# Performance work log

Hardware: AMD Instinct MI355X
Metric: run time of the kernel (lower is better)

Reference implementation:

```python
import jax, jax.numpy as jnp
import numpy as np

IN_CH = 256
BOT = IN_CH // 2  # bottleneck channels
B, W, H = 4, 64, 64


def setup_inputs() -> dict:
    key = jax.random.key(0)
    ks = jax.random.split(key, 10)
    s_in = 1.0 / np.sqrt(IN_CH)   # torch Conv2d default init scale (kaiming-ish bound)
    s_bt = 1.0 / np.sqrt(BOT)
    return {
        "X": jax.random.normal(ks[0], (B, IN_CH, W, H), dtype=jnp.float32),
        "Wq": jax.random.uniform(ks[1], (BOT, IN_CH), jnp.float32, -s_in, s_in),
        "bq": jax.random.uniform(ks[2], (BOT,), jnp.float32, -s_in, s_in),
        "Wk": jax.random.uniform(ks[3], (BOT, IN_CH), jnp.float32, -s_in, s_in),
        "bk": jax.random.uniform(ks[4], (BOT,), jnp.float32, -s_in, s_in),
        "Wv": jax.random.uniform(ks[5], (BOT, IN_CH), jnp.float32, -s_in, s_in),
        "bv": jax.random.uniform(ks[6], (BOT,), jnp.float32, -s_in, s_in),
        "Wo": jax.random.uniform(ks[7], (IN_CH, BOT), jnp.float32, -s_bt, s_bt),
        "bo": jax.random.uniform(ks[8], (IN_CH,), jnp.float32, -s_bt, s_bt),
        "gamma": 0.1 * jax.random.normal(ks[9], (1,), dtype=jnp.float32),
    }


def reference(X, Wq, bq, Wk, bk, Wv, bv, Wo, bo, gamma):
    b, c, w, h = X.shape
    n = w * h
    Xf = X.reshape(b, c, n)  # [b, c, n] — 1x1 conv == per-pixel linear
    q = jnp.einsum('oc,bcn->bon', Wq, Xf) + bq[None, :, None]  # [b, c/2, n]
    k = jnp.einsum('oc,bcn->bon', Wk, Xf) + bk[None, :, None]
    v = jnp.einsum('oc,bcn->bon', Wv, Xf) + bv[None, :, None]
    # score[b,i,j] = sum_c q[b,c,i] * k[b,c,j]; softmax over dim=1 (query index i)
    score = jnp.einsum('bci,bcj->bij', q, k)          # [b, n, n]
    attn = jax.nn.softmax(score, axis=1)
    out = jnp.einsum('bci,bij->bcj', v, attn)         # [b, c/2, n]
    out = jnp.einsum('oc,bcn->bon', Wo, out) + bo[None, :, None]  # [b, c, n]
    out = out.reshape(b, c, w, h)
    return gamma[0] * out + X
```

## Files before the change

### kernel.cpp

```cpp
#include <hip/hip_runtime.h>
#include <math.h>

#define NBATCH 4
#define CIN    256
#define CBOT   128
#define NPIX   4096
#define NPART  4
#define LOG2E  1.44269504f

typedef __attribute__((ext_vector_type(4))) float f32x4;
typedef __attribute__((ext_vector_type(8))) short bf16x8;

__device__ __forceinline__ unsigned short f2bf(float f) {
    union { float f; unsigned u; } v; v.f = f;
    unsigned r = (v.u + 0x7FFFu + ((v.u >> 16) & 1u)) >> 16;
    return (unsigned short)r;
}
__device__ __forceinline__ float bf2f(unsigned short h) {
    union { unsigned u; float f; } v; v.u = ((unsigned)h) << 16; return v.f;
}
__device__ __forceinline__ bf16x8 pack8(const float* s) {
    bf16x8 r;
#pragma unroll
    for (int t = 0; t < 8; ++t) r[t] = (short)f2bf(s[t]);
    return r;
}

__global__ __launch_bounds__(256) void k_xt(
    const float* __restrict__ X, unsigned short* __restrict__ Xt)
{
    __shared__ float T[64][65];
    const int tid = threadIdx.x;
    const int pbase = blockIdx.x * 64;
    const int c0    = blockIdx.y * 64;
    const int b     = blockIdx.z;
#pragma unroll
    for (int k = 0; k < 4; ++k) {
        int f = tid + 256 * k;
        int cl = f >> 4, p4 = (f & 15) << 2;
        float4 v = *(const float4*)(X + (size_t)b * CIN * NPIX + (size_t)(c0 + cl) * NPIX + pbase + p4);
        T[cl][p4 + 0] = v.x; T[cl][p4 + 1] = v.y;
        T[cl][p4 + 2] = v.z; T[cl][p4 + 3] = v.w;
    }
    __syncthreads();
#pragma unroll
    for (int k = 0; k < 4; ++k) {
        int f = tid + 256 * k;
        int p = f >> 4, c4 = (f & 15) << 2;
        ushort4 u;
        u.x = f2bf(T[c4 + 0][p]); u.y = f2bf(T[c4 + 1][p]);
        u.z = f2bf(T[c4 + 2][p]); u.w = f2bf(T[c4 + 3][p]);
        *(ushort4*)&Xt[((size_t)b * NPIX + pbase + p) * CIN + c0 + c4] = u;
    }
}

__global__ __launch_bounds__(256) void k_qkv(
    const unsigned short* __restrict__ Xt,
    const float* __restrict__ Wq, const float* __restrict__ bq,
    const float* __restrict__ Wk, const float* __restrict__ bk,
    const float* __restrict__ Wv, const float* __restrict__ bv,
    unsigned short* __restrict__ Qt, unsigned short* __restrict__ Kt,
    unsigned short* __restrict__ Vt)
{
    const int tid = threadIdx.x;
    const int wv = tid >> 6, lane = tid & 63;
    const int grp = lane & 15, quad = lane >> 4;
    const int pbase = blockIdx.x * 64;
    const int b     = blockIdx.y;
    const unsigned short* __restrict__ Xb = Xt + (size_t)b * NPIX * CIN;
    const int obase = 32 * wv;

    f32x4 aQ[2][4], aK[2][4], aV[4][2];
#pragma unroll
    for (int mt = 0; mt < 2; ++mt)
#pragma unroll
        for (int nt = 0; nt < 4; ++nt) { aQ[mt][nt] = (f32x4)0.f; aK[mt][nt] = (f32x4)0.f; }
#pragma unroll
    for (int mt = 0; mt < 4; ++mt)
#pragma unroll
        for (int nt = 0; nt < 2; ++nt) aV[mt][nt] = (f32x4)0.f;

    for (int ks = 0; ks < 8; ++ks) {
        bf16x8 bx[4];
#pragma unroll
        for (int nt = 0; nt < 4; ++nt)
            bx[nt] = *(const bf16x8*)&Xb[(size_t)(pbase + nt * 16 + grp) * CIN + ks * 32 + quad * 8];
        bf16x8 wq_[2], wk_[2], wv_[2];
#pragma unroll
        for (int mt = 0; mt < 2; ++mt) {
            const size_t roff = (size_t)(obase + mt * 16 + grp) * CIN + ks * 32 + quad * 8;
            float w8[8];
            *(float4*)&w8[0] = *(const float4*)(Wq + roff);
            *(float4*)&w8[4] = *(const float4*)(Wq + roff + 4);
            wq_[mt] = pack8(w8);
            *(float4*)&w8[0] = *(const float4*)(Wk + roff);
            *(float4*)&w8[4] = *(const float4*)(Wk + roff + 4);
            wk_[mt] = pack8(w8);
            *(float4*)&w8[0] = *(const float4*)(Wv + roff);
            *(float4*)&w8[4] = *(const float4*)(Wv + roff + 4);
            wv_[mt] = pack8(w8);
        }
#pragma unroll
        for (int mt = 0; mt < 2; ++mt)
#pragma unroll
            for (int nt = 0; nt < 4; ++nt) {
                aQ[mt][nt] = __builtin_amdgcn_mfma_f32_16x16x32_bf16(wq_[mt], bx[nt], aQ[mt][nt], 0, 0, 0);
                aK[mt][nt] = __builtin_amdgcn_mfma_f32_16x16x32_bf16(wk_[mt], bx[nt], aK[mt][nt], 0, 0, 0);
            }
#pragma unroll
        for (int mt = 0; mt < 4; ++mt)
#pragma unroll
            for (int nt = 0; nt < 2; ++nt)
                aV[mt][nt] = __builtin_amdgcn_mfma_f32_16x16x32_bf16(bx[mt], wv_[nt], aV[mt][nt], 0, 0, 0);
    }

    unsigned short* Qb_ = Qt + (size_t)b * NPIX * CBOT;
    unsigned short* Kb_ = Kt + (size_t)b * NPIX * CBOT;
#pragma unroll
    for (int mt = 0; mt < 2; ++mt) {
        int o0 = obase + mt * 16 + quad * 4;
        float b4q[4], b4k[4];
#pragma unroll
        for (int r = 0; r < 4; ++r) { b4q[r] = bq[o0 + r]; b4k[r] = bk[o0 + r]; }
#pragma unroll
        for (int nt = 0; nt < 4; ++nt) {
            int p = pbase + nt * 16 + grp;
            ushort4 uq, uk;
            uq.x = f2bf(aQ[mt][nt][0] + b4q[0]); uq.y = f2bf(aQ[mt][nt][1] + b4q[1]);
            uq.z = f2bf(aQ[mt][nt][2] + b4q[2]); uq.w = f2bf(aQ[mt][nt][3] + b4q[3]);
            uk.x = f2bf((aK[mt][nt][0] + b4k[0]) * LOG2E);
            uk.y = f2bf((aK[mt][nt][1] + b4k[1]) * LOG2E);
            uk.z = f2bf((aK[mt][nt][2] + b4k[2]) * LOG2E);
            uk.w = f2bf((aK[mt][nt][3] + b4k[3]) * LOG2E);
            *(ushort4*)&Qb_[(size_t)p * CBOT + o0] = uq;
            *(ushort4*)&Kb_[(size_t)p * CBOT + o0] = uk;
        }
    }
    unsigned short* Vb_ = Vt + (size_t)b * CBOT * NPIX;
#pragma unroll
    for (int nt = 0; nt < 2; ++nt) {
        int o = obase + nt * 16 + grp;
        float bb = bv[o];
#pragma unroll
        for (int mt = 0; mt < 4; ++mt) {
            int p0 = pbase + mt * 16 + quad * 4;
            ushort4 u;
            u.x = f2bf(aV[mt][nt][0] + bb); u.y = f2bf(aV[mt][nt][1] + bb);
            u.z = f2bf(aV[mt][nt][2] + bb); u.w = f2bf(aV[mt][nt][3] + bb);
            *(ushort4*)&Vb_[(size_t)o * NPIX + p0] = u;
        }
    }
}

__global__ __launch_bounds__(256, 2) void k_flash(
    const unsigned short* __restrict__ Qt,
    const unsigned short* __restrict__ Kt,
    const unsigned short* __restrict__ Vt,
    unsigned short* __restrict__ Opart,
    float* __restrict__ Lpart)
{
    __shared__ __align__(16) unsigned short Qs[64][136];
    __shared__ __align__(16) unsigned short Vs[128][72];
    __shared__ __align__(16) unsigned short Ps[128][72];
    const int tid  = threadIdx.x;
    const int wv   = tid >> 6, lane = tid & 63;
    const int grp  = lane & 15, quad = lane >> 4;
    const int jblk = blockIdx.x * 128;
    const int part = blockIdx.y;
    const int b    = blockIdx.z;
    const int tbeg = part * (64 / NPART);
    const int tend = tbeg + (64 / NPART);
    const unsigned short* __restrict__ Qb = Qt + (size_t)b * NPIX * CBOT;
    const unsigned short* __restrict__ Kb = Kt + (size_t)b * NPIX * CBOT;
    const unsigned short* __restrict__ Vb = Vt + (size_t)b * CBOT * NPIX;

    bf16x8 aq[2][4];
#pragma unroll
    for (int set = 0; set < 2; ++set)
#pragma unroll
        for (int ks = 0; ks < 4; ++ks)
            aq[set][ks] = *(const bf16x8*)&Kb[
                (size_t)(jblk + wv * 32 + set * 16 + grp) * CBOT + ks * 32 + quad * 8];

    bf16x8 bones;
#pragma unroll
    for (int t = 0; t < 8; ++t) bones[t] = (short)0x3F80;

    f32x4 o[2][8];
#pragma unroll
    for (int set = 0; set < 2; ++set)
#pragma unroll
        for (int ct = 0; ct < 8; ++ct) o[set][ct] = (f32x4)0.f;
    f32x4 lacc[2] = {(f32x4)0.f, (f32x4)0.f};

    const int qrow = tid >> 4,          qch = tid & 15;
    const int vrow = tid >> 3,          vch = tid & 7;
    bf16x8 qreg[4], vreg[4];
#pragma unroll
    for (int k = 0; k < 4; ++k) {
        qreg[k] = *(const bf16x8*)&Qb[(size_t)(tbeg * 64 + qrow + 16 * k) * CBOT + qch * 8];
        vreg[k] = *(const bf16x8*)&Vb[(size_t)(vrow + 32 * k) * NPIX + tbeg * 64 + vch * 8];
    }

    for (int it = tbeg; it < tend; ++it) {
        __syncthreads();
#pragma unroll
        for (int k = 0; k < 4; ++k) {
            *(bf16x8*)&Qs[qrow + 16 * k][qch * 8] = qreg[k];
            *(bf16x8*)&Vs[vrow + 32 * k][vch * 8] = vreg[k];
        }
        __syncthreads();
        if (it + 1 < tend) {
            const int i1 = (it + 1) * 64;
#pragma unroll
            for (int k = 0; k < 4; ++k) {
                qreg[k] = *(const bf16x8*)&Qb[(size_t)(i1 + qrow + 16 * k) * CBOT + qch * 8];
                vreg[k] = *(const bf16x8*)&Vb[(size_t)(vrow + 32 * k) * NPIX + i1 + vch * 8];
            }
        }

        f32x4 sf[2][4];
#pragma unroll
        for (int set = 0; set < 2; ++set)
#pragma unroll
            for (int nt = 0; nt < 4; ++nt) sf[set][nt] = (f32x4)0.f;
#pragma unroll
        for (int nt = 0; nt < 4; ++nt)
#pragma unroll
            for (int ks = 0; ks < 4; ++ks) {
                bf16x8 bq_ = *(const bf16x8*)&Qs[nt * 16 + grp][ks * 32 + quad * 8];
                sf[0][nt] = __builtin_amdgcn_mfma_f32_16x16x32_bf16(aq[0][ks], bq_, sf[0][nt], 0, 0, 0);
                sf[1][nt] = __builtin_amdgcn_mfma_f32_16x16x32_bf16(aq[1][ks], bq_, sf[1][nt], 0, 0, 0);
            }

#pragma unroll
        for (int set = 0; set < 2; ++set)
#pragma unroll
            for (int nt = 0; nt < 4; ++nt)
#pragma unroll
                for (int r = 0; r < 4; ++r)
                    Ps[wv * 32 + set * 16 + quad * 4 + r][nt * 16 + grp] =
                        f2bf(exp2f(sf[set][nt][r]));

        bf16x8 af[2][2];
#pragma unroll
        for (int set = 0; set < 2; ++set)
#pragma unroll
            for (int ks2 = 0; ks2 < 2; ++ks2)
                af[set][ks2] = *(const bf16x8*)&Ps[wv * 32 + set * 16 + grp][ks2 * 32 + quad * 8];

#pragma unroll
        for (int ct = 0; ct < 8; ++ct)
#pragma unroll
            for (int ks2 = 0; ks2 < 2; ++ks2) {
                bf16x8 bv_ = *(const bf16x8*)&Vs[ct * 16 + grp][ks2 * 32 + quad * 8];
                o[0][ct] = __builtin_amdgcn_mfma_f32_16x16x32_bf16(af[0][ks2], bv_, o[0][ct], 0, 0, 0);
                o[1][ct] = __builtin_amdgcn_mfma_f32_16x16x32_bf16(af[1][ks2], bv_, o[1][ct], 0, 0, 0);
            }
#pragma unroll
        for (int set = 0; set < 2; ++set) {
            lacc[set] = __builtin_amdgcn_mfma_f32_16x16x32_bf16(af[set][0], bones, lacc[set], 0, 0, 0);
            lacc[set] = __builtin_amdgcn_mfma_f32_16x16x32_bf16(af[set][1], bones, lacc[set], 0, 0, 0);
        }
    }

    unsigned short* Ob = Opart + ((size_t)(part * NBATCH + b) * NPIX + jblk) * CBOT;
#pragma unroll
    for (int set = 0; set < 2; ++set)
#pragma unroll
        for (int ct = 0; ct < 8; ++ct)
#pragma unroll
            for (int r = 0; r < 4; ++r)
                Ob[(size_t)(wv * 32 + set * 16 + quad * 4 + r) * CBOT + ct * 16 + grp] =
                    f2bf(o[set][ct][r]);
    if (grp == 0) {
#pragma unroll
        for (int set = 0; set < 2; ++set)
#pragma unroll
            for (int r = 0; r < 4; ++r)
                Lpart[(size_t)(part * NBATCH + b) * NPIX + jblk + wv * 32 + set * 16 + quad * 4 + r] =
                    lacc[set][r];
    }
}

__global__ __launch_bounds__(256) void k_oproj(
    const unsigned short* __restrict__ Opart, const float* __restrict__ Lpart,
    const float* __restrict__ Wo, const float* __restrict__ bo,
    const float* __restrict__ gamma, const float* __restrict__ X,
    float* __restrict__ Out)
{
    const int tid = threadIdx.x;
    const int wv = tid >> 6, lane = tid & 63;
    const int grp = lane & 15, quad = lane >> 4;
    const int pbase = blockIdx.x * 32;
    const int b     = blockIdx.y;
    const int obase = 64 * wv;

    f32x4 acc[2][4];
#pragma unroll
    for (int mt = 0; mt < 2; ++mt)
#pragma unroll
        for (int nt = 0; nt < 4; ++nt) acc[mt][nt] = (f32x4)0.f;

    for (int ks = 0; ks < 4; ++ks) {
        bf16x8 ao[2];
#pragma unroll
        for (int mt = 0; mt < 2; ++mt) {
            int p = pbase + mt * 16 + grp;
            float s[8] = {0.f, 0.f, 0.f, 0.f, 0.f, 0.f, 0.f, 0.f};
#pragma unroll
            for (int part = 0; part < NPART; ++part) {
                bf16x8 u = *(const bf16x8*)&Opart[
                    ((size_t)(part * NBATCH + b) * NPIX + p) * CBOT + ks * 32 + quad * 8];
#pragma unroll
                for (int t = 0; t < 8; ++t) s[t] += bf2f((unsigned short)u[t]);
            }
            ao[mt] = pack8(s);
        }
        bf16x8 bw[4];
#pragma unroll
        for (int nt = 0; nt < 4; ++nt) {
            const float* wp = Wo + (size_t)(obase + nt * 16 + grp) * CBOT + ks * 32 + quad * 8;
            float w8[8];
            *(float4*)&w8[0] = *(const float4*)wp;
            *(float4*)&w8[4] = *(const float4*)(wp + 4);
            bw[nt] = pack8(w8);
        }
#pragma unroll
        for (int mt = 0; mt < 2; ++mt)
#pragma unroll
            for (int nt = 0; nt < 4; ++nt)
                acc[mt][nt] = __builtin_amdgcn_mfma_f32_16x16x32_bf16(ao[mt], bw[nt], acc[mt][nt], 0, 0, 0);
    }

    float linv[2][4];
#pragma unroll
    for (int mt = 0; mt < 2; ++mt)
#pragma unroll
        for (int r = 0; r < 4; ++r) {
            int p = pbase + mt * 16 + quad * 4 + r;
            float ls = 0.f;
#pragma unroll
            for (int part = 0; part < NPART; ++part)
                ls += Lpart[(size_t)(part * NBATCH + b) * NPIX + p];
            linv[mt][r] = 1.f / ls;
        }
    float g = gamma[0];
#pragma unroll
    for (int nt = 0; nt < 4; ++nt) {
        int o = obase + nt * 16 + grp;
        float bb = bo[o];
#pragma unroll
        for (int mt = 0; mt < 2; ++mt) {
            int p0 = pbase + mt * 16 + quad * 4;
            size_t base = (size_t)b * CIN * NPIX + (size_t)o * NPIX + p0;
            float4 x4 = *(const float4*)(X + base);
            float4 r4;
            r4.x = g * (acc[mt][nt][0] * linv[mt][0] + bb) + x4.x;
            r4.y = g * (acc[mt][nt][1] * linv[mt][1] + bb) + x4.y;
            r4.z = g * (acc[mt][nt][2] * linv[mt][2] + bb) + x4.z;
            r4.w = g * (acc[mt][nt][3] * linv[mt][3] + bb) + x4.w;
            *(float4*)(Out + base) = r4;
        }
    }
}

extern "C" void kernel_launch(void* const* d_in, const int* in_sizes, int n_in,
                              void* d_out, int out_size, void* d_ws, size_t ws_size,
                              hipStream_t stream)
{
    (void)in_sizes; (void)n_in; (void)out_size; (void)ws_size;
    const float* X     = (const float*)d_in[0];
    const float* Wq    = (const float*)d_in[1];
    const float* bq    = (const float*)d_in[2];
    const float* Wk    = (const float*)d_in[3];
    const float* bk    = (const float*)d_in[4];
    const float* Wv    = (const float*)d_in[5];
    const float* bv    = (const float*)d_in[6];
    const float* Wo    = (const float*)d_in[7];
    const float* bo    = (const float*)d_in[8];
    const float* gamma = (const float*)d_in[9];
    float* out = (float*)d_out;

    const size_t BNC = (size_t)NBATCH * NPIX * CBOT;
    unsigned short* Qt    = (unsigned short*)d_ws;
    unsigned short* Kt    = Qt + BNC;
    unsigned short* Vt    = Kt + BNC;
    unsigned short* Opart = Vt + BNC;
    unsigned short* Xt    = Opart;
    float*          Lpart = (float*)(Opart + (size_t)NPART * BNC);

    k_xt   <<<dim3(64, 4, NBATCH),     256, 0, stream>>>(X, Xt);
    k_qkv  <<<dim3(64, NBATCH),        256, 0, stream>>>(Xt, Wq, bq, Wk, bk, Wv, bv, Qt, Kt, Vt);
    k_flash<<<dim3(32, NPART, NBATCH), 256, 0, stream>>>(Qt, Kt, Vt, Opart, Lpart);
    k_oproj<<<dim3(128, NBATCH),       256, 0, stream>>>(Opart, Lpart, Wo, bo, gamma, X, out);
}
```

Before: 177.1 us.

## Pre-convert weights to bf16 once, halve qkv pixel tile, skip partial summation

```diff
diff --git a/kernel.cpp b/kernel.cpp
--- a/kernel.cpp
+++ b/kernel.cpp
@@ -16,14 +16,21 @@
     unsigned r = (v.u + 0x7FFFu + ((v.u >> 16) & 1u)) >> 16;
     return (unsigned short)r;
 }
-__device__ __forceinline__ float bf2f(unsigned short h) {
-    union { unsigned u; float f; } v; v.u = ((unsigned)h) << 16; return v.f;
-}
-__device__ __forceinline__ bf16x8 pack8(const float* s) {
-    bf16x8 r;
-#pragma unroll
-    for (int t = 0; t < 8; ++t) r[t] = (short)f2bf(s[t]);
-    return r;
+
+__global__ __launch_bounds__(256) void k_wcvt(
+    const float* __restrict__ Wq, const float* __restrict__ Wk,
+    const float* __restrict__ Wv, const float* __restrict__ Wo,
+    unsigned short* __restrict__ Wb)
+{
+    const int f4 = (blockIdx.x * 256 + threadIdx.x) * 4;
+    const int reg = f4 >> 15, loc = f4 & 32767;
+    const float* __restrict__ W = (reg == 0) ? Wq : (reg == 1) ? Wk : (reg == 2) ? Wv : Wo;
+    const float sc = (reg == 1) ? LOG2E : 1.f;
+    float4 v = *(const float4*)(W + loc);
+    ushort4 u;
+    u.x = f2bf(v.x * sc); u.y = f2bf(v.y * sc);
+    u.z = f2bf(v.z * sc); u.w = f2bf(v.w * sc);
+    *(ushort4*)&Wb[f4] = u;
 }
 
 __global__ __launch_bounds__(256) void k_xt(
@@ -56,62 +63,52 @@
 
 __global__ __launch_bounds__(256) void k_qkv(
     const unsigned short* __restrict__ Xt,
-    const float* __restrict__ Wq, const float* __restrict__ bq,
-    const float* __restrict__ Wk, const float* __restrict__ bk,
-    const float* __restrict__ Wv, const float* __restrict__ bv,
+    const unsigned short* __restrict__ Wb,
+    const float* __restrict__ bq, const float* __restrict__ bk,
+    const float* __restrict__ bv,
     unsigned short* __restrict__ Qt, unsigned short* __restrict__ Kt,
     unsigned short* __restrict__ Vt)
 {
     const int tid = threadIdx.x;
     const int wv = tid >> 6, lane = tid & 63;
     const int grp = lane & 15, quad = lane >> 4;
-    const int pbase = blockIdx.x * 64;
+    const int pbase = blockIdx.x * 32;
     const int b     = blockIdx.y;
-    const unsigned short* __restrict__ Xb = Xt + (size_t)b * NPIX * CIN;
+    const unsigned short* __restrict__ Xb  = Xt + (size_t)b * NPIX * CIN;
+    const unsigned short* __restrict__ Wqb = Wb;
+    const unsigned short* __restrict__ Wkb = Wb + 32768;
+    const unsigned short* __restrict__ Wvb = Wb + 65536;
     const int obase = 32 * wv;
 
-    f32x4 aQ[2][4], aK[2][4], aV[4][2];
+    f32x4 aQ[2][2], aK[2][2], aV[2][2];
 #pragma unroll
     for (int mt = 0; mt < 2; ++mt)
 #pragma unroll
-        for (int nt = 0; nt < 4; ++nt) { aQ[mt][nt] = (f32x4)0.f; aK[mt][nt] = (f32x4)0.f; }
-#pragma unroll
-    for (int mt = 0; mt < 4; ++mt)
-#pragma unroll
-        for (int nt = 0; nt < 2; ++nt) aV[mt][nt] = (f32x4)0.f;
+        for (int nt = 0; nt < 2; ++nt) {
+            aQ[mt][nt] = (f32x4)0.f; aK[mt][nt] = (f32x4)0.f; aV[mt][nt] = (f32x4)0.f;
+        }
 
     for (int ks = 0; ks < 8; ++ks) {
-        bf16x8 bx[4];
-#pragma unroll
-        for (int nt = 0; nt < 4; ++nt)
+        bf16x8 bx[2];
+#pragma unroll
+        for (int nt = 0; nt < 2; ++nt)
             bx[nt] = *(const bf16x8*)&Xb[(size_t)(pbase + nt * 16 + grp) * CIN + ks * 32 + quad * 8];
         bf16x8 wq_[2], wk_[2], wv_[2];
 #pragma unroll
         for (int mt = 0; mt < 2; ++mt) {
             const size_t roff = (size_t)(obase + mt * 16 + grp) * CIN + ks * 32 + quad * 8;
-            float w8[8];
-            *(float4*)&w8[0] = *(const float4*)(Wq + roff);
-            *(float4*)&w8[4] = *(const float4*)(Wq + roff + 4);
-            wq_[mt] = pack8(w8);
-            *(float4*)&w8[0] = *(const float4*)(Wk + roff);
-            *(float4*)&w8[4] = *(const float4*)(Wk + roff + 4);
-            wk_[mt] = pack8(w8);
-            *(float4*)&w8[0] = *(const float4*)(Wv + roff);
-            *(float4*)&w8[4] = *(const float4*)(Wv + roff + 4);
-            wv_[mt] = pack8(w8);
+            wq_[mt] = *(const bf16x8*)&Wqb[roff];
+            wk_[mt] = *(const bf16x8*)&Wkb[roff];
+            wv_[mt] = *(const bf16x8*)&Wvb[roff];
         }
 #pragma unroll
         for (int mt = 0; mt < 2; ++mt)
 #pragma unroll
-            for (int nt = 0; nt < 4; ++nt) {
+            for (int nt = 0; nt < 2; ++nt) {
                 aQ[mt][nt] = __builtin_amdgcn_mfma_f32_16x16x32_bf16(wq_[mt], bx[nt], aQ[mt][nt], 0, 0, 0);
                 aK[mt][nt] = __builtin_amdgcn_mfma_f32_16x16x32_bf16(wk_[mt], bx[nt], aK[mt][nt], 0, 0, 0);
-            }
-#pragma unroll
-        for (int mt = 0; mt < 4; ++mt)
-#pragma unroll
-            for (int nt = 0; nt < 2; ++nt)
                 aV[mt][nt] = __builtin_amdgcn_mfma_f32_16x16x32_bf16(bx[mt], wv_[nt], aV[mt][nt], 0, 0, 0);
+            }
     }
 
     unsigned short* Qb_ = Qt + (size_t)b * NPIX * CBOT;
@@ -121,17 +118,15 @@
         int o0 = obase + mt * 16 + quad * 4;
         float b4q[4], b4k[4];
 #pragma unroll
-        for (int r = 0; r < 4; ++r) { b4q[r] = bq[o0 + r]; b4k[r] = bk[o0 + r]; }
-#pragma unroll
-        for (int nt = 0; nt < 4; ++nt) {
+        for (int r = 0; r < 4; ++r) { b4q[r] = bq[o0 + r]; b4k[r] = bk[o0 + r] * LOG2E; }
+#pragma unroll
+        for (int nt = 0; nt < 2; ++nt) {
             int p = pbase + nt * 16 + grp;
             ushort4 uq, uk;
             uq.x = f2bf(aQ[mt][nt][0] + b4q[0]); uq.y = f2bf(aQ[mt][nt][1] + b4q[1]);
             uq.z = f2bf(aQ[mt][nt][2] + b4q[2]); uq.w = f2bf(aQ[mt][nt][3] + b4q[3]);
-            uk.x = f2bf((aK[mt][nt][0] + b4k[0]) * LOG2E);
-            uk.y = f2bf((aK[mt][nt][1] + b4k[1]) * LOG2E);
-            uk.z = f2bf((aK[mt][nt][2] + b4k[2]) * LOG2E);
-            uk.w = f2bf((aK[mt][nt][3] + b4k[3]) * LOG2E);
+            uk.x = f2bf(aK[mt][nt][0] + b4k[0]); uk.y = f2bf(aK[mt][nt][1] + b4k[1]);
+            uk.z = f2bf(aK[mt][nt][2] + b4k[2]); uk.w = f2bf(aK[mt][nt][3] + b4k[3]);
             *(ushort4*)&Qb_[(size_t)p * CBOT + o0] = uq;
             *(ushort4*)&Kb_[(size_t)p * CBOT + o0] = uk;
         }
@@ -142,7 +137,7 @@
         int o = obase + nt * 16 + grp;
         float bb = bv[o];
 #pragma unroll
-        for (int mt = 0; mt < 4; ++mt) {
+        for (int mt = 0; mt < 2; ++mt) {
             int p0 = pbase + mt * 16 + quad * 4;
             ushort4 u;
             u.x = f2bf(aV[mt][nt][0] + bb); u.y = f2bf(aV[mt][nt][1] + bb);
@@ -193,8 +188,8 @@
         for (int ct = 0; ct < 8; ++ct) o[set][ct] = (f32x4)0.f;
     f32x4 lacc[2] = {(f32x4)0.f, (f32x4)0.f};
 
-    const int qrow = tid >> 4,          qch = tid & 15;
-    const int vrow = tid >> 3,          vch = tid & 7;
+    const int qrow = tid >> 4, qch = tid & 15;
+    const int vrow = tid >> 3, vch = tid & 7;
     bf16x8 qreg[4], vreg[4];
 #pragma unroll
     for (int k = 0; k < 4; ++k) {
@@ -285,7 +280,7 @@
 
 __global__ __launch_bounds__(256) void k_oproj(
     const unsigned short* __restrict__ Opart, const float* __restrict__ Lpart,
-    const float* __restrict__ Wo, const float* __restrict__ bo,
+    const unsigned short* __restrict__ Wob, const float* __restrict__ bo,
     const float* __restrict__ gamma, const float* __restrict__ X,
     float* __restrict__ Out)
 {
@@ -303,34 +298,22 @@
         for (int nt = 0; nt < 4; ++nt) acc[mt][nt] = (f32x4)0.f;
 
     for (int ks = 0; ks < 4; ++ks) {
-        bf16x8 ao[2];
+        bf16x8 bw[4];
+#pragma unroll
+        for (int nt = 0; nt < 4; ++nt)
+            bw[nt] = *(const bf16x8*)&Wob[(size_t)(obase + nt * 16 + grp) * CBOT + ks * 32 + quad * 8];
 #pragma unroll
         for (int mt = 0; mt < 2; ++mt) {
             int p = pbase + mt * 16 + grp;
-            float s[8] = {0.f, 0.f, 0.f, 0.f, 0.f, 0.f, 0.f, 0.f};
 #pragma unroll
             for (int part = 0; part < NPART; ++part) {
-                bf16x8 u = *(const bf16x8*)&Opart[
+                bf16x8 ao = *(const bf16x8*)&Opart[
                     ((size_t)(part * NBATCH + b) * NPIX + p) * CBOT + ks * 32 + quad * 8];
 #pragma unroll
-                for (int t = 0; t < 8; ++t) s[t] += bf2f((unsigned short)u[t]);
-            }
-            ao[mt] = pack8(s);
-        }
-        bf16x8 bw[4];
-#pragma unroll
-        for (int nt = 0; nt < 4; ++nt) {
-            const float* wp = Wo + (size_t)(obase + nt * 16 + grp) * CBOT + ks * 32 + quad * 8;
-            float w8[8];
-            *(float4*)&w8[0] = *(const float4*)wp;
-            *(float4*)&w8[4] = *(const float4*)(wp + 4);
-            bw[nt] = pack8(w8);
-        }
-#pragma unroll
-        for (int mt = 0; mt < 2; ++mt)
-#pragma unroll
-            for (int nt = 0; nt < 4; ++nt)
-                acc[mt][nt] = __builtin_amdgcn_mfma_f32_16x16x32_bf16(ao[mt], bw[nt], acc[mt][nt], 0, 0, 0);
+                for (int nt = 0; nt < 4; ++nt)
+                    acc[mt][nt] = __builtin_amdgcn_mfma_f32_16x16x32_bf16(ao, bw[nt], acc[mt][nt], 0, 0, 0);
+            }
+        }
     }
 
     float linv[2][4];
@@ -389,9 +372,11 @@
     unsigned short* Opart = Vt + BNC;
     unsigned short* Xt    = Opart;
     float*          Lpart = (float*)(Opart + (size_t)NPART * BNC);
-
+    unsigned short* Wb    = (unsigned short*)(Lpart + (size_t)NPART * NBATCH * NPIX);
+
+    k_wcvt <<<dim3(128),               256, 0, stream>>>(Wq, Wk, Wv, Wo, Wb);
     k_xt   <<<dim3(64, 4, NBATCH),     256, 0, stream>>>(X, Xt);
-    k_qkv  <<<dim3(64, NBATCH),        256, 0, stream>>>(Xt, Wq, bq, Wk, bk, Wv, bv, Qt, Kt, Vt);
+    k_qkv  <<<dim3(128, NBATCH),       256, 0, stream>>>(Xt, Wb, bq, bk, bv, Qt, Kt, Vt);
     k_flash<<<dim3(32, NPART, NBATCH), 256, 0, stream>>>(Qt, Kt, Vt, Opart, Lpart);
-    k_oproj<<<dim3(128, NBATCH),       256, 0, stream>>>(Opart, Lpart, Wo, bo, gamma, X, out);
-}
+    k_oproj<<<dim3(128, NBATCH),       256, 0, stream>>>(Opart, Lpart, Wb + 98304, bo, gamma, X, out);
+}
```

After: 174.5 us. About the same (-1.5%).
